# Optimization experiments

Measured on AMD Instinct MI355X. Metric: run time of the kernel, lower is better.

The kernel has to match this reference:

```python
import jax, jax.numpy as jnp
import numpy as np

VOCAB = 30
D_MODEL = 512
D_K = 64
D_V = 64
N_HEAD = 8
D_FF = 2048
N_LAYERS = 4
LN_EPS = 1e-5


def _make_pe(max_len, d_model):
    pos = np.arange(max_len, dtype=np.float32)[:, None]
    div = np.exp(np.arange(0, d_model, 2, dtype=np.float32) * (-np.log(10000.0) / d_model))
    pe = np.zeros((max_len, d_model), dtype=np.float32)
    pe[:, 0::2] = np.sin(pos * div)
    pe[:, 1::2] = np.cos(pos * div)
    return jnp.asarray(pe)


def setup_inputs() -> dict:
    key = jax.random.key(0)
    ks = jax.random.split(key, 16)
    B, S = 4, 2048
    s = 0.02
    inp = {
        "input_ids": jax.random.randint(ks[0], (B, S), 0, VOCAB, dtype=jnp.int64),
        "attn_mask": jax.random.randint(ks[1], (B, S), 0, 2, dtype=jnp.int64),
        "tok_embed": jax.random.normal(ks[2], (VOCAB, D_MODEL), jnp.float32) * s,
        "pe": _make_pe(S, D_MODEL),
        "Wq": jax.random.normal(ks[3], (N_LAYERS, D_MODEL, N_HEAD * D_K), jnp.float32) * s,
        "Wk": jax.random.normal(ks[4], (N_LAYERS, D_MODEL, N_HEAD * D_K), jnp.float32) * s,
        "Wv": jax.random.normal(ks[5], (N_LAYERS, D_MODEL, N_HEAD * D_V), jnp.float32) * s,
        "Wo": jax.random.normal(ks[6], (N_LAYERS, N_HEAD * D_V, D_MODEL), jnp.float32) * s,
        "ln1_g": jnp.ones((N_LAYERS, D_MODEL), jnp.float32),
        "ln1_b": jnp.zeros((N_LAYERS, D_MODEL), jnp.float32),
        "W1": jax.random.normal(ks[7], (N_LAYERS, D_MODEL, D_FF), jnp.float32) * s,
        "W2": jax.random.normal(ks[8], (N_LAYERS, D_FF, D_MODEL), jnp.float32) * s,
        "ln2_g": jnp.ones((N_LAYERS, D_MODEL), jnp.float32),
        "ln2_b": jnp.zeros((N_LAYERS, D_MODEL), jnp.float32),
    }
    return inp


def _layernorm(x, g, b):
    mu = jnp.mean(x, axis=-1, keepdims=True)
    var = jnp.mean(jnp.square(x - mu), axis=-1, keepdims=True)
    return (x - mu) * jax.lax.rsqrt(var + LN_EPS) * g + b


def reference(input_ids, attn_mask, tok_embed, pe, Wq, Wk, Wv, Wo, ln1_g, ln1_b, W1, W2, ln2_g, ln2_b):
    B, S = input_ids.shape
    x = tok_embed[input_ids] + pe[:S][None]  # [B,S,D]
    # pad mask: key positions where attn_mask==0, broadcast over heads & queries
    pad = (attn_mask == 0)[:, None, None, :]  # [B,1,1,S]
    scale = 1.0 / np.sqrt(D_K)
    for l in range(N_LAYERS):
        # multi-head self-attention
        q = (x @ Wq[l]).reshape(B, S, N_HEAD, D_K)
        k = (x @ Wk[l]).reshape(B, S, N_HEAD, D_K)
        v = (x @ Wv[l]).reshape(B, S, N_HEAD, D_V)
        scores = jnp.einsum('bqhd,bkhd->bhqk', q, k) * scale
        scores = jnp.where(pad, -1e9, scores)
        attn = jax.nn.softmax(scores, axis=-1)
        ctx = jnp.einsum('bhqk,bkhd->bqhd', attn, v).reshape(B, S, N_HEAD * D_V)
        x = _layernorm(ctx @ Wo[l] + x, ln1_g[l], ln1_b[l])
        # position-wise FFN
        h = jax.nn.relu(x @ W1[l])
        x = _layernorm(h @ W2[l] + x, ln2_g[l], ln2_b[l])
    return x
```

## Files before the change

kernel.cpp:

```cpp
#include <hip/hip_runtime.h>
#include <stdint.h>

#define S_LEN 2048
#define B_SZ 4
#define DM 512
#define NTOK (B_SZ * S_LEN)

typedef unsigned short u16;
typedef unsigned int u32;
typedef unsigned long long u64;
typedef __attribute__((ext_vector_type(8))) short short8;
typedef __attribute__((ext_vector_type(4))) float f32x4;

typedef const __attribute__((address_space(1))) u32 gq_t;
typedef __attribute__((address_space(3))) u32 lq_t;

__device__ __forceinline__ u16 f2bf(float f) {
  union { float f; u32 u; } v; v.f = f;
  return (u16)((v.u + 0x7FFFu + ((v.u >> 16) & 1u)) >> 16);
}

__device__ __forceinline__ float bf2f(u32 hi16_at_lo) {
  union { u32 u; float f; } v; v.u = hi16_at_lo;
  return v.f;
}

__device__ __forceinline__ float fexp2(float x) {
#if __has_builtin(__builtin_amdgcn_exp2f)
  return __builtin_amdgcn_exp2f(x);
#else
  return exp2f(x);
#endif
}

__device__ __forceinline__ short8 mk8(u64 a, u64 b) {
  union { u64 q[2]; short8 s; } u;
  u.q[0] = a; u.q[1] = b;
  return u.s;
}

__device__ __forceinline__ void swap32(u32& x, u32& y) {
  asm("v_permlane32_swap_b32 %0, %1" : "+v"(x), "+v"(y));
}
__device__ __forceinline__ void swap16(u32& x, u32& y, int lane) {
#if __has_builtin(__builtin_amdgcn_permlane16_swap)
  asm("v_permlane16_swap_b32 %0, %1" : "+v"(x), "+v"(y));
#else
  u32 tx = __builtin_amdgcn_ds_swizzle(x, 0x401F);
  u32 ty = __builtin_amdgcn_ds_swizzle(y, 0x401F);
  bool up = (lane & 16) != 0;
  u32 nx = up ? ty : x;
  u32 ny = up ? y : tx;
  x = nx; y = ny;
#endif
}

__global__ void compact_kernel(const int* __restrict__ mask, int* __restrict__ cidx,
                               int* __restrict__ cmap, int* __restrict__ nvalid) {
  __shared__ int wcnt[4];
  __shared__ int running;
  const int b = blockIdx.x, tid = threadIdx.x;
  if (tid == 0) running = 0;
  __syncthreads();
  for (int c = 0; c < 8; ++c) {
    int s = c * 256 + tid;
    int valid = (mask[b * 2048 + s] != 0) ? 1 : 0;
    u64 bal = __ballot(valid);
    int lane = tid & 63, wv = tid >> 6;
    int pre = __popcll(bal & ((1ULL << lane) - 1ULL));
    if (lane == 0) wcnt[wv] = __popcll(bal);
    __syncthreads();
    int woff = running;
    for (int j = 0; j < wv; ++j) woff += wcnt[j];
    int pos = woff + pre;
    if (valid) {
      cidx[b * 2048 + pos] = s;
      cmap[b * 2048 + s] = pos;
    } else {
      cmap[b * 2048 + s] = -1;
    }
    __syncthreads();
    if (tid == 0) running += wcnt[0] + wcnt[1] + wcnt[2] + wcnt[3];
    __syncthreads();
  }
  if (tid == 0) nvalid[b] = running;
}

__global__ void embed_kernel(const int* __restrict__ ids, const float* __restrict__ te,
                             const float* __restrict__ pe, u16* __restrict__ xb) {
  int gid = blockIdx.x * 256 + threadIdx.x;
  int tok = gid >> 7, c4 = (gid & 127) << 2;
  int s = tok & (S_LEN - 1);
  int id = ids[tok];
  const float4 a = *(const float4*)(te + (long)id * DM + c4);
  const float4 p = *(const float4*)(pe + (long)s * DM + c4);
  uint2 pk;
  pk.x = (u32)f2bf(a.x + p.x) | ((u32)f2bf(a.y + p.y) << 16);
  pk.y = (u32)f2bf(a.z + p.z) | ((u32)f2bf(a.w + p.w) << 16);
  *(uint2*)(xb + (long)tok * DM + c4) = pk;
}

__global__ void wconv_all(const float* __restrict__ Wq, const float* __restrict__ Wk,
                          const float* __restrict__ Wv, const float* __restrict__ Wo,
                          const float* __restrict__ W1, const float* __restrict__ W2,
                          u16* __restrict__ WqkvT, u16* __restrict__ WoT,
                          u16* __restrict__ W1T, u16* __restrict__ W2T) {
  __shared__ u16 t_lds[64 * 65];
  const int tile = blockIdx.x;
  const float* src; u16* dst; int N, K, kt, nt, l;
  if (tile < 768) {
    int which = tile >> 8, r = tile & 255;
    l = r >> 6; int rr = r & 63; kt = rr >> 3; nt = rr & 7;
    src = (which == 0 ? Wq : which == 1 ? Wk : Wv) + (long)l * 512 * 512;
    N = 512; K = 512;
    dst = WqkvT + (long)l * 1536 * 512 + (long)(which * 512) * 512;
  } else if (tile < 1024) {
    int r = tile - 768;
    l = r >> 6; int rr = r & 63; kt = rr >> 3; nt = rr & 7;
    src = Wo + (long)l * 512 * 512; N = 512; K = 512;
    dst = WoT + (long)l * 512 * 512;
  } else if (tile < 2048) {
    int r = tile - 1024;
    l = r >> 8; int rr = r & 255; kt = rr >> 5; nt = rr & 31;
    src = W1 + (long)l * 512 * 2048; N = 2048; K = 512;
    dst = W1T + (long)l * 2048 * 512;
  } else {
    int r = tile - 2048;
    l = r >> 8; int rr = r & 255; kt = rr >> 3; nt = rr & 7;
    src = W2 + (long)l * 2048 * 512; N = 512; K = 2048;
    dst = W2T + (long)l * 512 * 2048;
  }
  const int tr = threadIdx.x >> 4;
  const int tc = (threadIdx.x & 15) << 2;
#pragma unroll
  for (int i = 0; i < 4; ++i) {
    int k = tr + i * 16;
    const float4 v = *(const float4*)(src + (long)(kt * 64 + k) * N + nt * 64 + tc);
    t_lds[(tc + 0) * 65 + k] = f2bf(v.x);
    t_lds[(tc + 1) * 65 + k] = f2bf(v.y);
    t_lds[(tc + 2) * 65 + k] = f2bf(v.z);
    t_lds[(tc + 3) * 65 + k] = f2bf(v.w);
  }
  __syncthreads();
#pragma unroll
  for (int i = 0; i < 4; ++i) {
    int n = tr + i * 16;
    u16 a0 = t_lds[n * 65 + tc + 0];
    u16 a1 = t_lds[n * 65 + tc + 1];
    u16 a2 = t_lds[n * 65 + tc + 2];
    u16 a3 = t_lds[n * 65 + tc + 3];
    uint2 pk;
    pk.x = (u32)a0 | ((u32)a1 << 16);
    pk.y = (u32)a2 | ((u32)a3 << 16);
    *(uint2*)(dst + (long)(nt * 64 + n) * K + kt * 64 + tc) = pk;
  }
}

template <int BM, int BN, bool RELU, bool VSPLIT, bool SWAPC>
__global__ __launch_bounds__(BM * 2) void gemm_kernel(const u16* __restrict__ A,
                                                      const u16* __restrict__ BT,
                                                      void* __restrict__ Cout,
                                                      u16* __restrict__ vt,
                                                      const int* __restrict__ cmap,
                                                      int M, int N, int K) {
  constexpr int NI = BN / 32;
  constexpr int NW = BM / 32;
  constexpr int BRW = BN / NW;
  constexpr int LOADS = 4 + BRW / 8;
  __shared__ __align__(16) u16 a_t[2][BM * 64];
  __shared__ __align__(16) u16 b_t[2][BN * 64];
  const int tid = threadIdx.x;
  const int w = tid >> 6, lane = tid & 63;
  const int wr = w >> 1, wc = w & 1;
  const int g = lane >> 4, lr = lane & 15;
  const int l8 = lane >> 3, lch = lane & 7;
  const int gc = lch ^ l8;
  const int nwg = gridDim.x * gridDim.y;
  const int bid = blockIdx.x + gridDim.x * blockIdx.y;
  const int cpx = nwg >> 3;
  const int swz = (bid & 7) * cpx + (bid >> 3);
  const int bx = swz % gridDim.x, by = swz / gridDim.x;
  const long m0 = (long)by * BM, n0 = (long)bx * BN;
  f32x4 acc[4][NI] = {};
  const int nk = K >> 6;

  auto stage = [&](int nb, int kt) {
    const int k0 = kt << 6;
#pragma unroll
    for (int i = 0; i < 4; ++i) {
      int row = w * 32 + i * 8 + l8;
      __builtin_amdgcn_global_load_lds((gq_t*)(A + (m0 + row) * K + k0 + gc * 8),
                                       (lq_t*)&a_t[nb][(w * 4 + i) * 512], 16, 0, 0);
    }
#pragma unroll
    for (int i = 0; i < BRW / 8; ++i) {
      int row = w * BRW + i * 8 + l8;
      __builtin_amdgcn_global_load_lds((gq_t*)(BT + (n0 + row) * K + k0 + gc * 8),
                                       (lq_t*)&b_t[nb][(w * (BRW / 8) + i) * 512], 16, 0, 0);
    }
  };

  stage(0, 0);
  stage(1, 1);
  for (int kt = 0; kt < nk; ++kt) {
    const int cur = kt & 1;
    if (kt + 1 < nk) {
      if constexpr (LOADS == 6) asm volatile("s_waitcnt vmcnt(6)" ::: "memory");
      else                      asm volatile("s_waitcnt vmcnt(5)" ::: "memory");
    } else {
      asm volatile("s_waitcnt vmcnt(0)" ::: "memory");
    }
    __builtin_amdgcn_s_barrier();
    __builtin_amdgcn_sched_barrier(0);
    short8 af[2][4], bfr[2][NI];
#pragma unroll
    for (int ks = 0; ks < 2; ++ks) {
#pragma unroll
      for (int mi = 0; mi < 4; ++mi) {
        int row = wr * 64 + mi * 16 + lr;
        int byte = row * 128 + (((ks * 4 + g) ^ (row & 7)) << 4);
        af[ks][mi] = *(const short8*)((const char*)a_t[cur] + byte);
      }
#pragma unroll
      for (int ni = 0; ni < NI; ++ni) {
        int row = wc * (BN / 2) + ni * 16 + lr;
        int byte = row * 128 + (((ks * 4 + g) ^ (row & 7)) << 4);
        bfr[ks][ni] = *(const short8*)((const char*)b_t[cur] + byte);
      }
    }
    asm volatile("s_waitcnt lgkmcnt(0)" ::: "memory");
    __builtin_amdgcn_s_barrier();
    __builtin_amdgcn_sched_barrier(0);
    if (kt + 2 < nk) stage(cur, kt + 2);
    __builtin_amdgcn_s_setprio(1);
#pragma unroll
    for (int ks = 0; ks < 2; ++ks)
#pragma unroll
      for (int mi = 0; mi < 4; ++mi)
#pragma unroll
        for (int ni = 0; ni < NI; ++ni) {
          if constexpr (SWAPC)
            acc[mi][ni] = __builtin_amdgcn_mfma_f32_16x16x32_bf16(bfr[ks][ni], af[ks][mi], acc[mi][ni], 0, 0, 0);
          else
            acc[mi][ni] = __builtin_amdgcn_mfma_f32_16x16x32_bf16(af[ks][mi], bfr[ks][ni], acc[mi][ni], 0, 0, 0);
        }
    __builtin_amdgcn_s_setprio(0);
  }

  if constexpr (VSPLIT) {
    if (n0 >= 1024) {
#pragma unroll
      for (int mi = 0; mi < 4; ++mi) {
        long tok0 = m0 + wr * 64 + mi * 16 + g * 4;
#pragma unroll
        for (int j = 0; j < 4; ++j) {
          int cs = cmap[tok0 + j];
          if (cs < 0) continue;
          int bb = (int)((tok0 + j) >> 11);
#pragma unroll
          for (int ni = 0; ni < NI; ++ni) {
            int vc = (int)(n0 - 1024) + wc * (BN / 2) + ni * 16 + lr;
            int hh = vc >> 6, d = vc & 63;
            vt[(((long)bb * 8 + hh) * 64 + d) * 2048 + cs] = f2bf(acc[mi][ni][j]);
          }
        }
      }
      return;
    }
  }
  if constexpr (SWAPC) {
#pragma unroll
    for (int mi = 0; mi < 4; ++mi)
#pragma unroll
      for (int ni = 0; ni < NI; ++ni) {
        long grow = m0 + wr * 64 + mi * 16 + lr;
        long gcb = n0 + wc * (BN / 2) + ni * 16 + 4 * g;
        float v0 = acc[mi][ni][0], v1 = acc[mi][ni][1], v2 = acc[mi][ni][2], v3 = acc[mi][ni][3];
        if (RELU) {
          v0 = fmaxf(v0, 0.f); v1 = fmaxf(v1, 0.f); v2 = fmaxf(v2, 0.f); v3 = fmaxf(v3, 0.f);
        }
        uint2 pk;
        pk.x = (u32)f2bf(v0) | ((u32)f2bf(v1) << 16);
        pk.y = (u32)f2bf(v2) | ((u32)f2bf(v3) << 16);
        *(uint2*)((u16*)Cout + grow * N + gcb) = pk;
      }
  } else {
#pragma unroll
    for (int mi = 0; mi < 4; ++mi)
#pragma unroll
      for (int ni = 0; ni < NI; ++ni)
#pragma unroll
        for (int j = 0; j < 4; ++j) {
          long grow = m0 + wr * 64 + mi * 16 + g * 4 + j;
          long gcol = n0 + wc * (BN / 2) + ni * 16 + lr;
          float v = acc[mi][ni][j];
          if (RELU) v = fmaxf(v, 0.f);
          ((u16*)Cout)[grow * N + gcol] = f2bf(v);
        }
  }
}

__global__ __launch_bounds__(512) void attn_kernel(const u16* __restrict__ qkv,
                                                   const u16* __restrict__ vt,
                                                   const int* __restrict__ cidx,
                                                   const int* __restrict__ nvalid,
                                                   u16* __restrict__ ctx) {
  __shared__ __align__(16) u16 kv[2 * 4096 + 2 * 4096 + 1024];
  __shared__ __align__(16) float mvals[2][64];
  __shared__ __align__(16) float l_lds[128];
  const int tid = threadIdx.x;
  const int w = tid >> 6, lane = tid & 63;
  const int g = lane >> 4, lr = lane & 15;
  const int l8 = lane >> 3, lch = lane & 7;
  const int gc = lch ^ l8;
  const int b = blockIdx.z, h = blockIdx.y, q0 = blockIdx.x * 128;
  const long base = (long)b * S_LEN * 1536;
  const int qcol = h * 64, kcol = 512 + h * 64;
  const u16* vhead = vt + (((long)b * 8 + h) * 64) * 2048;
  u16* q_t = kv;
  u16* vone = kv + 16384;
  const float SC = 0.18033688011112042f;
  const int nv = nvalid[b];
  const int nt = (nv + 63) >> 6;

  auto stageKV = [&](int nb, int kb) {
    int kr = kb + w * 8 + l8;
    int cs = (kr < nv) ? cidx[b * 2048 + kr] : 0;
    __builtin_amdgcn_global_load_lds((gq_t*)(qkv + base + (long)cs * 1536 + kcol + gc * 8),
                                     (lq_t*)(kv + nb * 4096 + w * 512), 16, 0, 0);
    int row = w * 8 + l8;
    __builtin_amdgcn_global_load_lds((gq_t*)(vhead + (long)row * 2048 + kb + gc * 8),
                                     (lq_t*)(kv + 8192 + nb * 4096 + w * 512), 16, 0, 0);
    if (tid < 64) mvals[nb][tid] = (kb + tid < nv) ? 0.f : -1e9f;
  };

  {
    u32 val = ((tid >> 5) == 0) ? 0x3F803F80u : 0u;
    *(u32*)((char*)vone + tid * 4) = val;
  }
#pragma unroll
  for (int i = 0; i < 2; ++i) {
    int e = i * 512 + tid;
    int row = e >> 3, ch = e & 7;
    uint4 v = *(const uint4*)(qkv + base + (long)(q0 + row) * 1536 + qcol + ch * 8);
    *(uint4*)((char*)q_t + row * 128 + ((ch ^ (row & 7)) << 4)) = v;
  }
  __syncthreads();
  short8 qf[2];
#pragma unroll
  for (int ks = 0; ks < 2; ++ks) {
    int row = w * 16 + lr;
    qf[ks] = *(const short8*)((const char*)q_t + row * 128 + (((ks * 4 + g) ^ (row & 7)) << 4));
  }
  __syncthreads();
  stageKV(0, 0);
  __syncthreads();

  f32x4 o[5] = {};

  for (int kt = 0; kt < nt; ++kt) {
    const int cur = kt & 1;
    if (kt + 1 < nt) stageKV(cur ^ 1, (kt + 1) * 64);

    f32x4 s[4] = {};
    __builtin_amdgcn_s_setprio(1);
#pragma unroll
    for (int ks = 0; ks < 2; ++ks) {
#pragma unroll
      for (int ni = 0; ni < 4; ++ni) {
        int row = ni * 16 + lr;
        short8 kf = *(const short8*)((const char*)(kv + cur * 4096) + row * 128 + (((ks * 4 + g) ^ (row & 7)) << 4));
        s[ni] = __builtin_amdgcn_mfma_f32_16x16x32_bf16(kf, qf[ks], s[ni], 0, 0, 0);
      }
    }
    __builtin_amdgcn_s_setprio(0);
    float p[4][4];
#pragma unroll
    for (int ni = 0; ni < 4; ++ni) {
      const float4 mv = *(const float4*)&mvals[cur][ni * 16 + 4 * g];
      const float mva[4] = {mv.x, mv.y, mv.z, mv.w};
#pragma unroll
      for (int r = 0; r < 4; ++r)
        p[ni][r] = fexp2(fmaf(s[ni][r], SC, mva[r]));
    }
    u32 wv[4][2];
#pragma unroll
    for (int ni = 0; ni < 4; ++ni)
#pragma unroll
      for (int pp = 0; pp < 2; ++pp)
        asm("v_cvt_pk_bf16_f32 %0, %1, %2"
            : "=v"(wv[ni][pp]) : "v"(p[ni][2 * pp]), "v"(p[ni][2 * pp + 1]));

    u32 x0 = wv[0][0], x1 = wv[0][1], y0 = wv[1][0], y1 = wv[1][1];
    swap32(x0, y0); swap32(x1, y1);
    swap16(x0, y0, lane); swap16(x1, y1, lane);
    short8 pa0 = mk8((u64)x0 | ((u64)x1 << 32), (u64)y0 | ((u64)y1 << 32));
    u32 x2 = wv[2][0], x3 = wv[2][1], y2 = wv[3][0], y3 = wv[3][1];
    swap32(x2, y2); swap32(x3, y3);
    swap16(x2, y2, lane); swap16(x3, y3, lane);
    short8 pa1 = mk8((u64)x2 | ((u64)x3 << 32), (u64)y2 | ((u64)y3 << 32));

    __builtin_amdgcn_s_setprio(1);
#pragma unroll
    for (int ks2 = 0; ks2 < 2; ++ks2) {
      short8 pa = ks2 ? pa1 : pa0;
#pragma unroll
      for (int nd = 0; nd < 5; ++nd) {
        short8 vf;
        if (nd < 4) {
          int vrow = nd * 16 + lr;
          vf = *(const short8*)((const char*)(kv + 8192 + cur * 4096) + vrow * 128 + (((ks2 * 4 + g) ^ (vrow & 7)) << 4));
        } else {
          vf = *(const short8*)((const char*)vone + lr * 128 + (((ks2 * 4 + g) ^ (lr & 7)) << 4));
        }
        o[nd] = __builtin_amdgcn_mfma_f32_16x16x32_bf16(pa, vf, o[nd], 0, 0, 0);
      }
    }
    __builtin_amdgcn_s_setprio(0);
    if (kt + 1 < nt) __syncthreads();
  }
  if (lr == 0) {
#pragma unroll
    for (int r = 0; r < 4; ++r) l_lds[w * 16 + 4 * g + r] = o[4][r];
  }
  const float4 lv = *(const float4*)&l_lds[w * 16 + 4 * g];
  const float la[4] = {lv.x, lv.y, lv.z, lv.w};
  float inv[4];
#pragma unroll
  for (int r = 0; r < 4; ++r) inv[r] = 1.f / la[r];
#pragma unroll
  for (int nd = 0; nd < 4; ++nd)
#pragma unroll
    for (int r = 0; r < 4; ++r) {
      int tok = q0 + w * 16 + 4 * g + r;
      int col = h * 64 + nd * 16 + lr;
      ctx[((long)b * S_LEN + tok) * 512 + col] = f2bf(o[nd][r] * inv[r]);
    }
}

template <bool FINAL>
__global__ __launch_bounds__(256) void ln_kernel(const u16* __restrict__ y,
                                                 const u16* __restrict__ res,
                                                 const float* __restrict__ gam,
                                                 const float* __restrict__ bet,
                                                 u16* __restrict__ xout,
                                                 float* __restrict__ outf) {
  const int row = blockIdx.x, t = threadIdx.x;
  const long o0 = (long)row * DM;
  const u32 yb = *(const u32*)(y + o0 + 2 * t);
  const u32 rb = *(const u32*)(res + o0 + 2 * t);
  float a0 = bf2f(yb << 16) + bf2f(rb << 16);
  float a1 = bf2f(yb & 0xFFFF0000u) + bf2f(rb & 0xFFFF0000u);
  float s1 = a0 + a1, s2 = a0 * a0 + a1 * a1;
#pragma unroll
  for (int m = 32; m >= 1; m >>= 1) {
    s1 += __shfl_xor(s1, m);
    s2 += __shfl_xor(s2, m);
  }
  __shared__ float w1[4], w2[4];
  if ((t & 63) == 0) { w1[t >> 6] = s1; w2[t >> 6] = s2; }
  __syncthreads();
  s1 = w1[0] + w1[1] + w1[2] + w1[3];
  s2 = w2[0] + w2[1] + w2[2] + w2[3];
  const float mu = s1 * (1.f / DM);
  const float rstd = rsqrtf(s2 * (1.f / DM) - mu * mu + 1e-5f);
  const float2 gv = *(const float2*)&gam[2 * t];
  const float2 bv = *(const float2*)&bet[2 * t];
  float r0 = (a0 - mu) * rstd * gv.x + bv.x;
  float r1 = (a1 - mu) * rstd * gv.y + bv.y;
  if constexpr (FINAL) {
    float2 ov; ov.x = r0; ov.y = r1;
    *(float2*)&outf[o0 + 2 * t] = ov;
  } else {
    u32 pk = (u32)f2bf(r0) | ((u32)f2bf(r1) << 16);
    *(u32*)&xout[o0 + 2 * t] = pk;
  }
}

extern "C" void kernel_launch(void* const* d_in, const int* in_sizes, int n_in,
                              void* d_out, int out_size, void* d_ws, size_t ws_size,
                              hipStream_t stream) {
  const int*   ids  = (const int*)d_in[0];
  const int*   amsk = (const int*)d_in[1];
  const float* te   = (const float*)d_in[2];
  const float* pe   = (const float*)d_in[3];
  const float* Wq   = (const float*)d_in[4];
  const float* Wk   = (const float*)d_in[5];
  const float* Wv   = (const float*)d_in[6];
  const float* Wo   = (const float*)d_in[7];
  const float* ln1g = (const float*)d_in[8];
  const float* ln1b = (const float*)d_in[9];
  const float* W1   = (const float*)d_in[10];
  const float* W2   = (const float*)d_in[11];
  const float* ln2g = (const float*)d_in[12];
  const float* ln2b = (const float*)d_in[13];
  float* out = (float*)d_out;

  char* p = (char*)d_ws;
  u16* x     = (u16*)p;   p += (long)NTOK * DM * 2;
  u16* qkv   = (u16*)p;   p += (long)NTOK * 1536 * 2;
  u16* ctx   = (u16*)p;   p += (long)NTOK * DM * 2;
  u16* tmp   = (u16*)p;   p += (long)NTOK * DM * 2;
  u16* hb    = (u16*)p;   p += (long)NTOK * 2048 * 2;
  u16* WqkvT = (u16*)p;   p += (long)4 * 1536 * 512 * 2;
  u16* WoT   = (u16*)p;   p += (long)4 * 512 * 512 * 2;
  u16* W1T   = (u16*)p;   p += (long)4 * 2048 * 512 * 2;
  u16* W2T   = (u16*)p;   p += (long)4 * 512 * 2048 * 2;
  int* cidx  = (int*)p;   p += (long)B_SZ * S_LEN * 4;
  int* cmap  = (int*)p;   p += (long)B_SZ * S_LEN * 4;
  int* nval  = (int*)p;   p += 64;
  if ((size_t)(p - (char*)d_ws) > ws_size) return;
  u16* vt = hb;

  compact_kernel<<<B_SZ, 256, 0, stream>>>(amsk, cidx, cmap, nval);
  wconv_all<<<3072, 256, 0, stream>>>(Wq, Wk, Wv, Wo, W1, W2, WqkvT, WoT, W1T, W2T);
  embed_kernel<<<NTOK * 128 / 256, 256, 0, stream>>>(ids, te, pe, x);

  for (int l = 0; l < 4; ++l) {
    gemm_kernel<256, 64, false, true, false><<<dim3(1536 / 64, NTOK / 256), 512, 0, stream>>>(
        x, WqkvT + (long)l * 1536 * 512, qkv, vt, cmap, NTOK, 1536, 512);
    attn_kernel<<<dim3(S_LEN / 128, 8, B_SZ), 512, 0, stream>>>(qkv, vt, cidx, nval, ctx);
    gemm_kernel<128, 64, false, false, true><<<dim3(512 / 64, NTOK / 128), 256, 0, stream>>>(
        ctx, WoT + (long)l * 512 * 512, tmp, nullptr, nullptr, NTOK, 512, 512);
    ln_kernel<false><<<NTOK, 256, 0, stream>>>(tmp, x, ln1g + l * 512, ln1b + l * 512, x, nullptr);
    gemm_kernel<256, 64, true, false, true><<<dim3(2048 / 64, NTOK / 256), 512, 0, stream>>>(
        x, W1T + (long)l * 2048 * 512, hb, nullptr, nullptr, NTOK, 2048, 512);
    gemm_kernel<128, 64, false, false, true><<<dim3(512 / 64, NTOK / 128), 256, 0, stream>>>(
        hb, W2T + (long)l * 512 * 2048, tmp, nullptr, nullptr, NTOK, 512, 2048);
    if (l == 3)
      ln_kernel<true><<<NTOK, 256, 0, stream>>>(tmp, x, ln2g + l * 512, ln2b + l * 512, nullptr, out);
    else
      ln_kernel<false><<<NTOK, 256, 0, stream>>>(tmp, x, ln2g + l * 512, ln2b + l * 512, x, nullptr);
  }
}
```

Baseline: 559.8 us.

## Project K/V only for unmasked tokens into compacted per-head buffers

```diff
diff --git a/kernel.cpp b/kernel.cpp
--- a/kernel.cpp
+++ b/kernel.cpp
@@ -56,7 +56,7 @@
 }
 
 __global__ void compact_kernel(const int* __restrict__ mask, int* __restrict__ cidx,
-                               int* __restrict__ cmap, int* __restrict__ nvalid) {
+                               int* __restrict__ nvalid) {
   __shared__ int wcnt[4];
   __shared__ int running;
   const int b = blockIdx.x, tid = threadIdx.x;
@@ -72,13 +72,7 @@
     __syncthreads();
     int woff = running;
     for (int j = 0; j < wv; ++j) woff += wcnt[j];
-    int pos = woff + pre;
-    if (valid) {
-      cidx[b * 2048 + pos] = s;
-      cmap[b * 2048 + s] = pos;
-    } else {
-      cmap[b * 2048 + s] = -1;
-    }
+    if (valid) cidx[b * 2048 + woff + pre] = s;
     __syncthreads();
     if (tid == 0) running += wcnt[0] + wcnt[1] + wcnt[2] + wcnt[3];
     __syncthreads();
@@ -156,12 +150,10 @@
   }
 }
 
-template <int BM, int BN, bool RELU, bool VSPLIT, bool SWAPC>
+template <int BM, int BN, bool RELU, bool SWAPC>
 __global__ __launch_bounds__(BM * 2) void gemm_kernel(const u16* __restrict__ A,
                                                       const u16* __restrict__ BT,
                                                       void* __restrict__ Cout,
-                                                      u16* __restrict__ vt,
-                                                      const int* __restrict__ cmap,
                                                       int M, int N, int K) {
   constexpr int NI = BN / 32;
   constexpr int NW = BM / 32;
@@ -247,27 +239,6 @@
     __builtin_amdgcn_s_setprio(0);
   }
 
-  if constexpr (VSPLIT) {
-    if (n0 >= 1024) {
-#pragma unroll
-      for (int mi = 0; mi < 4; ++mi) {
-        long tok0 = m0 + wr * 64 + mi * 16 + g * 4;
-#pragma unroll
-        for (int j = 0; j < 4; ++j) {
-          int cs = cmap[tok0 + j];
-          if (cs < 0) continue;
-          int bb = (int)((tok0 + j) >> 11);
-#pragma unroll
-          for (int ni = 0; ni < NI; ++ni) {
-            int vc = (int)(n0 - 1024) + wc * (BN / 2) + ni * 16 + lr;
-            int hh = vc >> 6, d = vc & 63;
-            vt[(((long)bb * 8 + hh) * 64 + d) * 2048 + cs] = f2bf(acc[mi][ni][j]);
-          }
-        }
-      }
-      return;
-    }
-  }
   if constexpr (SWAPC) {
 #pragma unroll
     for (int mi = 0; mi < 4; ++mi)
@@ -300,9 +271,130 @@
   }
 }
 
-__global__ __launch_bounds__(512) void attn_kernel(const u16* __restrict__ qkv,
+__global__ __launch_bounds__(512) void kvproj_kernel(const u16* __restrict__ x,
+                                                     const u16* __restrict__ BT,
+                                                     const int* __restrict__ cidx,
+                                                     const int* __restrict__ nvalid,
+                                                     u16* __restrict__ kcomp,
+                                                     u16* __restrict__ vt) {
+  __shared__ __align__(16) u16 a_t[2][256 * 64];
+  __shared__ __align__(16) u16 b_t[2][64 * 64];
+  const int tid = threadIdx.x;
+  const int w = tid >> 6, lane = tid & 63;
+  const int wr = w >> 1, wc = w & 1;
+  const int g = lane >> 4, lr = lane & 15;
+  const int l8 = lane >> 3, lch = lane & 7;
+  const int gc = lch ^ l8;
+  const int n0 = blockIdx.x * 64;
+  const int b = blockIdx.y >> 3, mt = blockIdx.y & 7;
+  const int nv = nvalid[b];
+  const int m0 = mt * 256;
+  if (m0 >= nv) return;
+  const bool isK = (n0 < 512);
+
+  long aoff[4];
+#pragma unroll
+  for (int i = 0; i < 4; ++i) {
+    int cr = m0 + w * 32 + i * 8 + l8;
+    int s = cidx[b * 2048 + (cr < nv ? cr : nv - 1)];
+    aoff[i] = ((long)b * 2048 + s) * 512;
+  }
+  f32x4 acc[4][2] = {};
+
+  auto stage = [&](int nb, int kt) {
+    const int k0 = kt << 6;
+#pragma unroll
+    for (int i = 0; i < 4; ++i)
+      __builtin_amdgcn_global_load_lds((gq_t*)(x + aoff[i] + k0 + gc * 8),
+                                       (lq_t*)&a_t[nb][(w * 4 + i) * 512], 16, 0, 0);
+    {
+      int row = n0 + w * 8 + l8;
+      __builtin_amdgcn_global_load_lds((gq_t*)(BT + (long)row * 512 + k0 + gc * 8),
+                                       (lq_t*)&b_t[nb][w * 512], 16, 0, 0);
+    }
+  };
+
+  stage(0, 0);
+  stage(1, 1);
+  for (int kt = 0; kt < 8; ++kt) {
+    const int cur = kt & 1;
+    if (kt + 1 < 8) asm volatile("s_waitcnt vmcnt(5)" ::: "memory");
+    else            asm volatile("s_waitcnt vmcnt(0)" ::: "memory");
+    __builtin_amdgcn_s_barrier();
+    __builtin_amdgcn_sched_barrier(0);
+    short8 af[2][4], bfr[2][2];
+#pragma unroll
+    for (int ks = 0; ks < 2; ++ks) {
+#pragma unroll
+      for (int mi = 0; mi < 4; ++mi) {
+        int row = wr * 64 + mi * 16 + lr;
+        int byte = row * 128 + (((ks * 4 + g) ^ (row & 7)) << 4);
+        af[ks][mi] = *(const short8*)((const char*)a_t[cur] + byte);
+      }
+#pragma unroll
+      for (int ni = 0; ni < 2; ++ni) {
+        int row = wc * 32 + ni * 16 + lr;
+        int byte = row * 128 + (((ks * 4 + g) ^ (row & 7)) << 4);
+        bfr[ks][ni] = *(const short8*)((const char*)b_t[cur] + byte);
+      }
+    }
+    asm volatile("s_waitcnt lgkmcnt(0)" ::: "memory");
+    __builtin_amdgcn_s_barrier();
+    __builtin_amdgcn_sched_barrier(0);
+    if (kt + 2 < 8) stage(cur, kt + 2);
+    __builtin_amdgcn_s_setprio(1);
+    if (isK) {
+#pragma unroll
+      for (int ks = 0; ks < 2; ++ks)
+#pragma unroll
+        for (int mi = 0; mi < 4; ++mi)
+#pragma unroll
+          for (int ni = 0; ni < 2; ++ni)
+            acc[mi][ni] = __builtin_amdgcn_mfma_f32_16x16x32_bf16(bfr[ks][ni], af[ks][mi], acc[mi][ni], 0, 0, 0);
+    } else {
+#pragma unroll
+      for (int ks = 0; ks < 2; ++ks)
+#pragma unroll
+        for (int mi = 0; mi < 4; ++mi)
+#pragma unroll
+          for (int ni = 0; ni < 2; ++ni)
+            acc[mi][ni] = __builtin_amdgcn_mfma_f32_16x16x32_bf16(af[ks][mi], bfr[ks][ni], acc[mi][ni], 0, 0, 0);
+    }
+    __builtin_amdgcn_s_setprio(0);
+  }
+
+  if (isK) {
+    const int h = n0 >> 6;
+#pragma unroll
+    for (int mi = 0; mi < 4; ++mi)
+#pragma unroll
+      for (int ni = 0; ni < 2; ++ni) {
+        long cr = m0 + wr * 64 + mi * 16 + lr;
+        int c = wc * 32 + ni * 16 + 4 * g;
+        uint2 pk;
+        pk.x = (u32)f2bf(acc[mi][ni][0]) | ((u32)f2bf(acc[mi][ni][1]) << 16);
+        pk.y = (u32)f2bf(acc[mi][ni][2]) | ((u32)f2bf(acc[mi][ni][3]) << 16);
+        *(uint2*)(kcomp + (((long)b * 8 + h) * 2048 + cr) * 64 + c) = pk;
+      }
+  } else {
+    const int h = (n0 - 512) >> 6;
+#pragma unroll
+    for (int mi = 0; mi < 4; ++mi)
+#pragma unroll
+      for (int ni = 0; ni < 2; ++ni) {
+        int d = wc * 32 + ni * 16 + lr;
+        long cr0 = m0 + wr * 64 + mi * 16 + g * 4;
+        uint2 pk;
+        pk.x = (u32)f2bf(acc[mi][ni][0]) | ((u32)f2bf(acc[mi][ni][1]) << 16);
+        pk.y = (u32)f2bf(acc[mi][ni][2]) | ((u32)f2bf(acc[mi][ni][3]) << 16);
+        *(uint2*)(vt + (((long)b * 8 + h) * 64 + d) * 2048 + cr0) = pk;
+      }
+  }
+}
+
+__global__ __launch_bounds__(512) void attn_kernel(const u16* __restrict__ qbuf,
+                                                   const u16* __restrict__ kcomp,
                                                    const u16* __restrict__ vt,
-                                                   const int* __restrict__ cidx,
                                                    const int* __restrict__ nvalid,
                                                    u16* __restrict__ ctx) {
   __shared__ __align__(16) u16 kv[2 * 4096 + 2 * 4096 + 1024];
@@ -314,8 +406,7 @@
   const int l8 = lane >> 3, lch = lane & 7;
   const int gc = lch ^ l8;
   const int b = blockIdx.z, h = blockIdx.y, q0 = blockIdx.x * 128;
-  const long base = (long)b * S_LEN * 1536;
-  const int qcol = h * 64, kcol = 512 + h * 64;
+  const u16* khead = kcomp + (((long)b * 8 + h) * 2048) * 64;
   const u16* vhead = vt + (((long)b * 8 + h) * 64) * 2048;
   u16* q_t = kv;
   u16* vone = kv + 16384;
@@ -324,11 +415,9 @@
   const int nt = (nv + 63) >> 6;
 
   auto stageKV = [&](int nb, int kb) {
-    int kr = kb + w * 8 + l8;
-    int cs = (kr < nv) ? cidx[b * 2048 + kr] : 0;
-    __builtin_amdgcn_global_load_lds((gq_t*)(qkv + base + (long)cs * 1536 + kcol + gc * 8),
+    int row = w * 8 + l8;
+    __builtin_amdgcn_global_load_lds((gq_t*)(khead + (long)(kb + row) * 64 + gc * 8),
                                      (lq_t*)(kv + nb * 4096 + w * 512), 16, 0, 0);
-    int row = w * 8 + l8;
     __builtin_amdgcn_global_load_lds((gq_t*)(vhead + (long)row * 2048 + kb + gc * 8),
                                      (lq_t*)(kv + 8192 + nb * 4096 + w * 512), 16, 0, 0);
     if (tid < 64) mvals[nb][tid] = (kb + tid < nv) ? 0.f : -1e9f;
@@ -342,7 +431,7 @@
   for (int i = 0; i < 2; ++i) {
     int e = i * 512 + tid;
     int row = e >> 3, ch = e & 7;
-    uint4 v = *(const uint4*)(qkv + base + (long)(q0 + row) * 1536 + qcol + ch * 8);
+    uint4 v = *(const uint4*)(qbuf + ((long)b * 2048 + q0 + row) * 512 + h * 64 + ch * 8);
     *(uint4*)((char*)q_t + row * 128 + ((ch ^ (row & 7)) << 4)) = v;
   }
   __syncthreads();
@@ -498,7 +587,8 @@
 
   char* p = (char*)d_ws;
   u16* x     = (u16*)p;   p += (long)NTOK * DM * 2;
-  u16* qkv   = (u16*)p;   p += (long)NTOK * 1536 * 2;
+  u16* qbuf  = (u16*)p;   p += (long)NTOK * DM * 2;
+  u16* kcomp = (u16*)p;   p += (long)B_SZ * 8 * 2048 * 64 * 2;
   u16* ctx   = (u16*)p;   p += (long)NTOK * DM * 2;
   u16* tmp   = (u16*)p;   p += (long)NTOK * DM * 2;
   u16* hb    = (u16*)p;   p += (long)NTOK * 2048 * 2;
@@ -507,26 +597,27 @@
   u16* W1T   = (u16*)p;   p += (long)4 * 2048 * 512 * 2;
   u16* W2T   = (u16*)p;   p += (long)4 * 512 * 2048 * 2;
   int* cidx  = (int*)p;   p += (long)B_SZ * S_LEN * 4;
-  int* cmap  = (int*)p;   p += (long)B_SZ * S_LEN * 4;
   int* nval  = (int*)p;   p += 64;
   if ((size_t)(p - (char*)d_ws) > ws_size) return;
   u16* vt = hb;
 
-  compact_kernel<<<B_SZ, 256, 0, stream>>>(amsk, cidx, cmap, nval);
+  compact_kernel<<<B_SZ, 256, 0, stream>>>(amsk, cidx, nval);
   wconv_all<<<3072, 256, 0, stream>>>(Wq, Wk, Wv, Wo, W1, W2, WqkvT, WoT, W1T, W2T);
   embed_kernel<<<NTOK * 128 / 256, 256, 0, stream>>>(ids, te, pe, x);
 
   for (int l = 0; l < 4; ++l) {
-    gemm_kernel<256, 64, false, true, false><<<dim3(1536 / 64, NTOK / 256), 512, 0, stream>>>(
-        x, WqkvT + (long)l * 1536 * 512, qkv, vt, cmap, NTOK, 1536, 512);
-    attn_kernel<<<dim3(S_LEN / 128, 8, B_SZ), 512, 0, stream>>>(qkv, vt, cidx, nval, ctx);
-    gemm_kernel<128, 64, false, false, true><<<dim3(512 / 64, NTOK / 128), 256, 0, stream>>>(
-        ctx, WoT + (long)l * 512 * 512, tmp, nullptr, nullptr, NTOK, 512, 512);
+    gemm_kernel<256, 64, false, true><<<dim3(512 / 64, NTOK / 256), 512, 0, stream>>>(
+        x, WqkvT + (long)l * 1536 * 512, qbuf, NTOK, 512, 512);
+    kvproj_kernel<<<dim3(16, 32), 512, 0, stream>>>(
+        x, WqkvT + (long)l * 1536 * 512 + (long)512 * 512, cidx, nval, kcomp, vt);
+    attn_kernel<<<dim3(S_LEN / 128, 8, B_SZ), 512, 0, stream>>>(qbuf, kcomp, vt, nval, ctx);
+    gemm_kernel<128, 64, false, true><<<dim3(512 / 64, NTOK / 128), 256, 0, stream>>>(
+        ctx, WoT + (long)l * 512 * 512, tmp, NTOK, 512, 512);
     ln_kernel<false><<<NTOK, 256, 0, stream>>>(tmp, x, ln1g + l * 512, ln1b + l * 512, x, nullptr);
-    gemm_kernel<256, 64, true, false, true><<<dim3(2048 / 64, NTOK / 256), 512, 0, stream>>>(
-        x, W1T + (long)l * 2048 * 512, hb, nullptr, nullptr, NTOK, 2048, 512);
-    gemm_kernel<128, 64, false, false, true><<<dim3(512 / 64, NTOK / 128), 256, 0, stream>>>(
-        hb, W2T + (long)l * 512 * 2048, tmp, nullptr, nullptr, NTOK, 512, 2048);
+    gemm_kernel<256, 64, true, true><<<dim3(2048 / 64, NTOK / 256), 512, 0, stream>>>(
+        x, W1T + (long)l * 2048 * 512, hb, NTOK, 2048, 512);
+    gemm_kernel<128, 64, false, true><<<dim3(512 / 64, NTOK / 128), 256, 0, stream>>>(
+        hb, W2T + (long)l * 512 * 2048, tmp, NTOK, 512, 2048);
     if (l == 3)
       ln_kernel<true><<<NTOK, 256, 0, stream>>>(tmp, x, ln2g + l * 512, ln2b + l * 512, nullptr, out);
     else
```

Result: no change. 564.0 us (+0.8%).
